# Optimization experiments

Measured on AMD Instinct MI355X. Metric: run time of the kernel, lower is better.

Reference implementation:

```python
import jax, jax.numpy as jnp
import numpy as np

T, D, N, K, H = 2048, 4096, 32, 8, 128
ROPE_THETA = 500000.0


def setup_inputs() -> dict:
    key = jax.random.key(0)
    ks = jax.random.split(key, 5)
    s = 0.02
    return {
        "x": jax.random.normal(ks[0], (T, D), jnp.float32) * s,
        "positions": jnp.arange(T, dtype=jnp.int64 if jax.config.jax_enable_x64 else jnp.int32),
        "Wq": jax.random.normal(ks[1], (D, N, H), jnp.float32) * s,
        "Wk": jax.random.normal(ks[2], (D, K, H), jnp.float32) * s,
        "Wv": jax.random.normal(ks[3], (D, K, H), jnp.float32) * s,
        "Wo": jax.random.normal(ks[4], (N, H, D), jnp.float32) * s,
    }


def _rope(positions, q, k):
    # positions: [T]; q: [T,N,H]; k: [T,K,H]. Half-split rotation (Llama style).
    half = H // 2
    inv_freq = 1.0 / (ROPE_THETA ** (jnp.arange(0, half, dtype=jnp.float32) / half))
    ang = positions.astype(jnp.float32)[:, None] * inv_freq  # [T, H/2]
    cos = jnp.cos(ang)[:, None, :]  # [T,1,H/2]
    sin = jnp.sin(ang)[:, None, :]

    def rot(x):
        x1, x2 = x[..., :half], x[..., half:]
        return jnp.concatenate([x1 * cos - x2 * sin, x2 * cos + x1 * sin], axis=-1)

    return rot(q), rot(k)


def reference(x, positions, Wq, Wk, Wv, Wo):
    q = jnp.einsum('td,dnh->tnh', x, Wq)  # [T,N,H]
    k = jnp.einsum('td,dkh->tkh', x, Wk)  # [T,K,H]
    v = jnp.einsum('td,dkh->tkh', x, Wv)
    q, k = _rope(positions, q, k)

    rep = N // K  # GQA: expand kv heads to query heads
    kr = jnp.repeat(k, rep, axis=1)  # [T,N,H]
    vr = jnp.repeat(v, rep, axis=1)

    scale = 1.0 / jnp.sqrt(jnp.asarray(H, jnp.float32))
    scores = jnp.einsum('tnh,snh->nts', q, kr) * scale  # [N,T,T]
    causal = positions[:, None] >= positions[None, :]   # [T,T]
    scores = jnp.where(causal[None, :, :], scores, jnp.finfo(scores.dtype).min)
    probs = jax.nn.softmax(scores, axis=-1)
    ctx = jnp.einsum('nts,snh->tnh', probs, vr)  # [T,N,H]
    return jnp.einsum('tnh,nhd->td', ctx, Wo)
```

## Files before the change

### kernel.cpp

```cpp
#include <hip/hip_runtime.h>
#include <hip/hip_bf16.h>

#define T_SEQ 2048
#define D_MODEL 4096
#define N_HEADS 32
#define K_HEADS 8
#define HEAD_DIM 128

typedef unsigned short u16;
typedef short sfrag8 __attribute__((ext_vector_type(8)));
typedef float ffrag4 __attribute__((ext_vector_type(4)));

#if defined(__has_builtin)
#  if __has_builtin(__builtin_amdgcn_exp2f)
#    define EXP2F(x) __builtin_amdgcn_exp2f(x)
#  else
#    define EXP2F(x) exp2f(x)
#  endif
#else
#  define EXP2F(x) exp2f(x)
#endif

#define QSCALE_LOG2E 0.12751744900463627f

__device__ __forceinline__ float bf2f(u16 u) {
    return __uint_as_float(((unsigned int)u) << 16);
}
__device__ __forceinline__ u16 f2bf(float f) {
    unsigned int x = __float_as_uint(f);
    unsigned int r = (x + 0x7fffu + ((x >> 16) & 1u)) >> 16;
    return (u16)r;
}
__device__ __forceinline__ uint4 pack8(const float4 a, const float4 b) {
    uint4 r;
    r.x = (unsigned)f2bf(a.x) | ((unsigned)f2bf(a.y) << 16);
    r.y = (unsigned)f2bf(a.z) | ((unsigned)f2bf(a.w) << 16);
    r.z = (unsigned)f2bf(b.x) | ((unsigned)f2bf(b.y) << 16);
    r.w = (unsigned)f2bf(b.z) | ((unsigned)f2bf(b.w) << 16);
    return r;
}

__device__ __forceinline__ void gload_lds16(const u16* g, u16* l) {
    __builtin_amdgcn_global_load_lds(
        (const __attribute__((address_space(1))) void*)g,
        (__attribute__((address_space(3))) void*)l, 16, 0, 0);
}

__global__ __launch_bounds__(256) void convert_bf16(
    const float* __restrict__ X, u16* __restrict__ Y, int n8)
{
    const int i = blockIdx.x * 256 + threadIdx.x;
    if (i < n8) {
        float4 a = ((const float4*)X)[(size_t)i * 2];
        float4 b = ((const float4*)X)[(size_t)i * 2 + 1];
        ((uint4*)Y)[i] = pack8(a, b);
    }
}

__global__ __launch_bounds__(256) void transpose_f32_bf16(
    const float* __restrict__ W, u16* __restrict__ WT, int R, int C)
{
    __shared__ float Ts[64][65];
    const int t = threadIdx.x;
    const int c0 = blockIdx.x * 64, r0 = blockIdx.y * 64;
    const int rl = t >> 4, cl = (t & 15) * 4;
#pragma unroll
    for (int p = 0; p < 4; ++p) {
        const int r = p * 16 + rl;
        float4 v = *(const float4*)(W + (size_t)(r0 + r) * C + c0 + cl);
        Ts[r][cl] = v.x; Ts[r][cl + 1] = v.y; Ts[r][cl + 2] = v.z; Ts[r][cl + 3] = v.w;
    }
    __syncthreads();
    const int nl = t >> 2, k4 = (t & 3) * 16;
    u16 tmp[16];
#pragma unroll
    for (int j = 0; j < 16; ++j) tmp[j] = f2bf(Ts[k4 + j][nl]);
    u16* dst = WT + (size_t)(c0 + nl) * R + r0 + k4;
    *(uint4*)(dst) = *(uint4*)&tmp[0];
    *(uint4*)(dst + 8) = *(uint4*)&tmp[8];
}

template <int CMODE>
__global__ __launch_bounds__(256) void gemm_bt(
    const u16* __restrict__ A, const u16* __restrict__ BT,
    void* __restrict__ Cp, int M, int Nb, int Kd, int ldc)
{
    __shared__ __align__(16) u16 As[128 * 64];
    __shared__ __align__(16) u16 Bs[128 * 64];

    const int tid = threadIdx.x;
    const int lane = tid & 63;
    const int w = tid >> 6;
    const int wm = w >> 1, wn = w & 1;
    const int ln = lane & 15, quad = lane >> 4;

    const int m0 = blockIdx.y * 128, n0 = blockIdx.x * 128;

    size_t aoff[4], boff[4];
#pragma unroll
    for (int i = 0; i < 4; ++i) {
        const int row = (i * 4 + w) * 8 + (lane >> 3);
        const int cg = (lane & 7) ^ (lane >> 3);
        aoff[i] = (size_t)(m0 + row) * Kd + cg * 8;
        boff[i] = (size_t)(n0 + row) * Kd + cg * 8;
    }

    ffrag4 acc[4][4];
#pragma unroll
    for (int mi = 0; mi < 4; ++mi)
#pragma unroll
        for (int ni = 0; ni < 4; ++ni) acc[mi][ni] = (ffrag4){0.f, 0.f, 0.f, 0.f};

    for (int k0 = 0; k0 < Kd; k0 += 64) {
#pragma unroll
        for (int i = 0; i < 4; ++i) {
            gload_lds16(A + aoff[i] + k0, &As[(i * 4 + w) * 512]);
            gload_lds16(BT + boff[i] + k0, &Bs[(i * 4 + w) * 512]);
        }
        __syncthreads();

#pragma unroll
        for (int kk = 0; kk < 2; ++kk) {
            sfrag8 af[4], bfv[4];
#pragma unroll
            for (int mi = 0; mi < 4; ++mi) {
                const int row = wm * 64 + mi * 16 + ln;
                const int pc = ((kk * 4) | quad) ^ (ln & 7);
                af[mi] = *(const sfrag8*)&As[row * 64 + pc * 8];
            }
#pragma unroll
            for (int ni = 0; ni < 4; ++ni) {
                const int row = wn * 64 + ni * 16 + ln;
                const int pc = ((kk * 4) | quad) ^ (ln & 7);
                bfv[ni] = *(const sfrag8*)&Bs[row * 64 + pc * 8];
            }
#pragma unroll
            for (int mi = 0; mi < 4; ++mi)
#pragma unroll
                for (int ni = 0; ni < 4; ++ni)
                    acc[mi][ni] = __builtin_amdgcn_mfma_f32_16x16x32_bf16(
                        af[mi], bfv[ni], acc[mi][ni], 0, 0, 0);
        }
        __syncthreads();
    }

#pragma unroll
    for (int mi = 0; mi < 4; ++mi) {
#pragma unroll
        for (int ni = 0; ni < 4; ++ni) {
            const int gcol = n0 + wn * 64 + ni * 16 + ln;
#pragma unroll
            for (int i = 0; i < 4; ++i) {
                const int grow = m0 + wm * 64 + mi * 16 + quad * 4 + i;
                if constexpr (CMODE == 1) {
                    ((float*)Cp)[(size_t)grow * ldc + gcol] = acc[mi][ni][i];
                } else if constexpr (CMODE == 3) {
                    if (gcol < 1024) {
                        ((u16*)Cp)[(size_t)grow * 1024 + gcol] = f2bf(acc[mi][ni][i]);
                    } else {
                        ((u16*)Cp + 2097152)[(size_t)(gcol - 1024) * T_SEQ + grow] =
                            f2bf(acc[mi][ni][i]);
                    }
                } else {
                    ((u16*)Cp)[(size_t)grow * ldc + gcol] = f2bf(acc[mi][ni][i]);
                }
            }
        }
    }
}

template <int AMODE, int CMODE>
__global__ __launch_bounds__(256) void gemm_any(
    const void* __restrict__ Ap, const float* __restrict__ B, void* __restrict__ Cp,
    int M, int Nb, int Kd, int ldc)
{
    __shared__ __align__(16) u16 As[64 * 64];
    __shared__ __align__(16) u16 Bs[64 * 72];

    const int tid = threadIdx.x;
    const int n0 = blockIdx.x * 64, m0 = blockIdx.y * 64;

    const int lr = tid >> 3;
    const int cc8 = tid & 7;
    const int sw = ((cc8 ^ (lr & 7)) * 8);
    const int dstA0 = lr * 64 + sw;
    const int dstA1 = (lr + 32) * 64 + sw;
    const size_t arow0 = (size_t)(m0 + lr) * Kd;
    const size_t arow1 = (size_t)(m0 + lr + 32) * Kd;

    const int kr = tid >> 2;
    const int ncb = (tid & 3) * 16;

    const int lane = tid & 63;
    const int w = tid >> 6;
    const int col16 = lane & 15;
    const int quad = lane >> 4;
    const int swl = lane & 7;
    const int mrow = w * 16 + col16;

    ffrag4 acc[4];
#pragma unroll
    for (int j = 0; j < 4; ++j) acc[j] = (ffrag4){0.f, 0.f, 0.f, 0.f};

    for (int k0 = 0; k0 < Kd; k0 += 64) {
        if constexpr (AMODE == 1) {
            const u16* Af = (const u16*)Ap;
            uint4 va0 = *(const uint4*)(Af + arow0 + k0 + cc8 * 8);
            uint4 va1 = *(const uint4*)(Af + arow1 + k0 + cc8 * 8);
            *(uint4*)&As[dstA0] = va0;
            *(uint4*)&As[dstA1] = va1;
        } else {
            const float* Af = (const float*)Ap;
            float4 a00 = *(const float4*)(Af + arow0 + k0 + cc8 * 8);
            float4 a01 = *(const float4*)(Af + arow0 + k0 + cc8 * 8 + 4);
            float4 a10 = *(const float4*)(Af + arow1 + k0 + cc8 * 8);
            float4 a11 = *(const float4*)(Af + arow1 + k0 + cc8 * 8 + 4);
            *(uint4*)&As[dstA0] = pack8(a00, a01);
            *(uint4*)&As[dstA1] = pack8(a10, a11);
        }
        {
            const float* bp = B + (size_t)(k0 + kr) * Nb + n0 + ncb;
            float4 b0 = *(const float4*)(bp);
            float4 b1 = *(const float4*)(bp + 4);
            float4 b2 = *(const float4*)(bp + 8);
            float4 b3 = *(const float4*)(bp + 12);
            u16 tmp[16];
            tmp[0] = f2bf(b0.x); tmp[1] = f2bf(b0.y); tmp[2] = f2bf(b0.z); tmp[3] = f2bf(b0.w);
            tmp[4] = f2bf(b1.x); tmp[5] = f2bf(b1.y); tmp[6] = f2bf(b1.z); tmp[7] = f2bf(b1.w);
            tmp[8] = f2bf(b2.x); tmp[9] = f2bf(b2.y); tmp[10] = f2bf(b2.z); tmp[11] = f2bf(b2.w);
            tmp[12] = f2bf(b3.x); tmp[13] = f2bf(b3.y); tmp[14] = f2bf(b3.z); tmp[15] = f2bf(b3.w);
#pragma unroll
            for (int e = 0; e < 16; ++e)
                Bs[(ncb + e) * 72 + kr] = tmp[e];
        }
        __syncthreads();
#pragma unroll
        for (int c = 0; c < 2; ++c) {
            const int cc = c * 4 + quad;
            const int koffA = (cc ^ swl) * 8;
            sfrag8 af = *(const sfrag8*)&As[mrow * 64 + koffA];
#pragma unroll
            for (int j = 0; j < 4; ++j) {
                sfrag8 bfv = *(const sfrag8*)&Bs[(j * 16 + col16) * 72 + cc * 8];
                acc[j] = __builtin_amdgcn_mfma_f32_16x16x32_bf16(af, bfv, acc[j], 0, 0, 0);
            }
        }
        __syncthreads();
    }

#pragma unroll
    for (int j = 0; j < 4; ++j) {
        const int gcol = n0 + j * 16 + col16;
#pragma unroll
        for (int i = 0; i < 4; ++i) {
            const int grow = m0 + w * 16 + quad * 4 + i;
            if constexpr (CMODE == 1) {
                ((float*)Cp)[(size_t)grow * ldc + gcol] = acc[j][i];
            } else if constexpr (CMODE == 2) {
                ((u16*)Cp)[(size_t)gcol * ldc + grow] = f2bf(acc[j][i]);
            } else {
                ((u16*)Cp)[(size_t)grow * ldc + gcol] = f2bf(acc[j][i]);
            }
        }
    }
}

__global__ __launch_bounds__(64) void rope_kernel(
    u16* __restrict__ buf, int nheads, int t0)
{
    const int h = blockIdx.x;
    const int t = blockIdx.y;
    u16* rowp = buf + ((size_t)t * nheads + h) * HEAD_DIM;
    const int i = threadIdx.x;
    const float p = (float)(t0 + t);
    const float inv = expf(-((float)i * (1.0f / 64.0f)) * 13.122363377404329f);
    const float ang = p * inv;
    const float c = cosf(ang);
    const float s = sinf(ang);
    const float x1 = bf2f(rowp[i]);
    const float x2 = bf2f(rowp[i + 64]);
    rowp[i] = f2bf(x1 * c - x2 * s);
    rowp[i + 64] = f2bf(x2 * c + x1 * s);
}

__global__ __launch_bounds__(256) void attn_mfma(
    const u16* q, const u16* __restrict__ k,
    const u16* __restrict__ vt, u16* ctx, int t0)
{
    __shared__ __align__(16) u16 Kt[64 * 136];
    __shared__ __align__(16) u16 Vt[128 * 72];
    __shared__ __align__(16) u16 Ps[4][16 * 72];

    const int head = blockIdx.x;
    const int qt = gridDim.y - 1 - blockIdx.y;
    const int kvh = head >> 2;
    const int tid = threadIdx.x;
    const int lane = tid & 63;
    const int w = tid >> 6;
    const int ln = lane & 15;
    const int quad = lane >> 4;

    const int kr = tid >> 2;
    const int c4 = (tid & 3) * 32;
    const int vd = tid >> 1;
    const int vh = (tid & 1) * 32;

    const int qrow_loc = qt * 64 + w * 16 + ln;
    sfrag8 qf[4];
    {
        const u16* qg = q + ((size_t)qrow_loc * N_HEADS + head) * HEAD_DIM;
#pragma unroll
        for (int kk = 0; kk < 4; ++kk)
            qf[kk] = *(const sfrag8*)(qg + kk * 32 + quad * 8);
    }

    ffrag4 acc_o[8];
#pragma unroll
    for (int dt = 0; dt < 8; ++dt) acc_o[dt] = (ffrag4){0.f, 0.f, 0.f, 0.f};
    float mrow[4] = {-INFINITY, -INFINITY, -INFINITY, -INFINITY};
    float lrow_l[4] = {0.f, 0.f, 0.f, 0.f};

    const int Tq0 = t0 + qt * 64;
    const int nst = Tq0 / 64 + 1;
    const int qabs_base = Tq0 + w * 16 + quad * 4;

    for (int st = 0; st < nst; ++st) {
        const int kv0 = st * 64;
        const bool diag = (st == nst - 1);

        __syncthreads();
        {
            const u16* kg = k + ((size_t)(kv0 + kr) * K_HEADS + kvh) * HEAD_DIM + c4;
            u16* kd = &Kt[kr * 136 + c4];
#pragma unroll
            for (int j = 0; j < 4; ++j)
                *(uint4*)(kd + j * 8) = *(const uint4*)(kg + j * 8);
        }
        {
            const u16* vg = vt + ((size_t)(kvh * 128 + vd)) * T_SEQ + kv0 + vh;
            u16* vdst = &Vt[vd * 72 + vh];
#pragma unroll
            for (int j = 0; j < 4; ++j)
                *(uint4*)(vdst + j * 8) = *(const uint4*)(vg + j * 8);
        }
        __syncthreads();

        const int ktc = diag ? ((w < 2) ? 2 : 4) : 4;
        ffrag4 sacc[4];
        __builtin_amdgcn_s_setprio(1);
#pragma unroll
        for (int kt = 0; kt < 4; ++kt) {
            if (kt >= ktc) break;
            sacc[kt] = (ffrag4){0.f, 0.f, 0.f, 0.f};
#pragma unroll
            for (int kk = 0; kk < 4; ++kk) {
                sfrag8 bfr = *(const sfrag8*)&Kt[(kt * 16 + ln) * 136 + kk * 32 + quad * 8];
                sacc[kt] = __builtin_amdgcn_mfma_f32_16x16x32_bf16(qf[kk], bfr, sacc[kt], 0, 0, 0);
            }
        }
        __builtin_amdgcn_s_setprio(0);
        float sv[4][4];
#pragma unroll
        for (int kt = 0; kt < 4; ++kt) {
            if (kt >= ktc) break;
            const int key_abs = kv0 + kt * 16 + ln;
#pragma unroll
            for (int i = 0; i < 4; ++i) {
                float s = sacc[kt][i] * QSCALE_LOG2E;
                if (diag && key_abs > qabs_base + i) s = -INFINITY;
                sv[kt][i] = s;
            }
        }
        float tm[4];
#pragma unroll
        for (int i = 0; i < 4; ++i) {
            float t = sv[0][i];
            for (int kt = 1; kt < ktc; ++kt) t = fmaxf(t, sv[kt][i]);
            t = fmaxf(t, __shfl_xor(t, 1));
            t = fmaxf(t, __shfl_xor(t, 2));
            t = fmaxf(t, __shfl_xor(t, 4));
            t = fmaxf(t, __shfl_xor(t, 8));
            tm[i] = t;
        }
        float alpha[4];
#pragma unroll
        for (int i = 0; i < 4; ++i) {
            const float mn = fmaxf(mrow[i], tm[i]);
            alpha[i] = EXP2F(mrow[i] - mn);
            mrow[i] = mn;
        }
        const bool noop = (alpha[0] == 1.f) && (alpha[1] == 1.f) &&
                          (alpha[2] == 1.f) && (alpha[3] == 1.f);
        if (!__all(noop)) {
#pragma unroll
            for (int i = 0; i < 4; ++i) {
                lrow_l[i] *= alpha[i];
#pragma unroll
                for (int dt = 0; dt < 8; ++dt) acc_o[dt][i] *= alpha[i];
            }
        }
#pragma unroll
        for (int kt = 0; kt < 4; ++kt) {
            if (kt >= ktc) break;
#pragma unroll
            for (int i = 0; i < 4; ++i) {
                const float p = EXP2F(sv[kt][i] - mrow[i]);
                lrow_l[i] += p;
                Ps[w][(quad * 4 + i) * 72 + kt * 16 + ln] = f2bf(p);
            }
        }
        const int kbm = ktc >> 1;
        __builtin_amdgcn_s_setprio(1);
#pragma unroll
        for (int kb = 0; kb < 2; ++kb) {
            if (kb >= kbm) break;
            sfrag8 afr = *(const sfrag8*)&Ps[w][ln * 72 + kb * 32 + quad * 8];
#pragma unroll
            for (int dt = 0; dt < 8; ++dt) {
                sfrag8 bfr = *(const sfrag8*)&Vt[(dt * 16 + ln) * 72 + kb * 32 + quad * 8];
                acc_o[dt] = __builtin_amdgcn_mfma_f32_16x16x32_bf16(afr, bfr, acc_o[dt], 0, 0, 0);
            }
        }
        __builtin_amdgcn_s_setprio(0);
    }

    float invl[4];
#pragma unroll
    for (int i = 0; i < 4; ++i) {
        float t = lrow_l[i];
        t += __shfl_xor(t, 1);
        t += __shfl_xor(t, 2);
        t += __shfl_xor(t, 4);
        t += __shfl_xor(t, 8);
        invl[i] = 1.0f / t;
    }
#pragma unroll
    for (int i = 0; i < 4; ++i) {
        u16* og = ctx + ((size_t)(qt * 64 + w * 16 + quad * 4 + i) * N_HEADS + head) * HEAD_DIM;
#pragma unroll
        for (int dt = 0; dt < 8; ++dt)
            og[dt * 16 + ln] = f2bf(acc_o[dt][i] * invl[i]);
    }
}

extern "C" void kernel_launch(void* const* d_in, const int* in_sizes, int n_in,
                              void* d_out, int out_size, void* d_ws, size_t ws_size,
                              hipStream_t stream) {
    (void)in_sizes; (void)n_in; (void)out_size;
    const float* x  = (const float*)d_in[0];
    const float* Wq = (const float*)d_in[2];
    const float* Wk = (const float*)d_in[3];
    const float* Wv = (const float*)d_in[4];
    const float* Wo = (const float*)d_in[5];
    float* out = (float*)d_out;
    char* ws = (char*)d_ws;
    const size_t MiB = 1024 * 1024;

    if (ws_size >= 88 * MiB) {
        u16* kbuf  = (u16*)(ws);
        u16* vtbuf = (u16*)(ws + 4 * MiB);
        u16* qsl   = (u16*)(ws + 8 * MiB);
        u16* xb    = (u16*)(ws + 24 * MiB);
        u16* WkT   = (u16*)(ws + 40 * MiB);
        u16* WvT   = (u16*)(ws + 48 * MiB);
        u16* WshT  = (u16*)(ws + 56 * MiB);

        convert_bf16<<<dim3(T_SEQ * D_MODEL / 8 / 256), 256, 0, stream>>>(
            x, xb, T_SEQ * D_MODEL / 8);
        transpose_f32_bf16<<<dim3(16, 64), 256, 0, stream>>>(
            Wk, WkT, D_MODEL, K_HEADS * HEAD_DIM);
        transpose_f32_bf16<<<dim3(16, 64), 256, 0, stream>>>(
            Wv, WvT, D_MODEL, K_HEADS * HEAD_DIM);
        transpose_f32_bf16<<<dim3(64, 64), 256, 0, stream>>>(
            Wq, WshT, D_MODEL, N_HEADS * HEAD_DIM);

        gemm_bt<3><<<dim3(16, 16), 256, 0, stream>>>(
            xb, WkT, kbuf, T_SEQ, 2048, D_MODEL, 0);
        rope_kernel<<<dim3(K_HEADS, T_SEQ), 64, 0, stream>>>(kbuf, K_HEADS, 0);

        gemm_bt<0><<<dim3(32, 16), 256, 0, stream>>>(
            xb, WshT, qsl, T_SEQ, N_HEADS * HEAD_DIM, D_MODEL, N_HEADS * HEAD_DIM);
        rope_kernel<<<dim3(N_HEADS, T_SEQ), 64, 0, stream>>>(qsl, N_HEADS, 0);

        attn_mfma<<<dim3(N_HEADS, T_SEQ / 64), 256, 0, stream>>>(
            qsl, kbuf, vtbuf, qsl, 0);

        transpose_f32_bf16<<<dim3(64, 64), 256, 0, stream>>>(
            Wo, WshT, N_HEADS * HEAD_DIM, D_MODEL);
        gemm_bt<1><<<dim3(32, 16), 256, 0, stream>>>(
            qsl, WshT, out, T_SEQ, D_MODEL, N_HEADS * HEAD_DIM, D_MODEL);
        return;
    }

    u16* kbuf  = (u16*)(ws);
    u16* vtbuf = (u16*)(ws + 4194304);
    u16* qsl   = (u16*)(ws + 8388608);

    int S = 8;
    if (ws_size >= (size_t)8388608 + 16777216)      S = 1;
    else if (ws_size >= (size_t)8388608 + 8388608)  S = 2;
    else if (ws_size >= (size_t)8388608 + 4194304)  S = 4;
    const int Ts = T_SEQ / S;

    gemm_any<0, 0><<<dim3(16, T_SEQ / 64), 256, 0, stream>>>(
        x, Wk, kbuf, T_SEQ, K_HEADS * HEAD_DIM, D_MODEL, K_HEADS * HEAD_DIM);
    gemm_any<0, 2><<<dim3(16, T_SEQ / 64), 256, 0, stream>>>(
        x, Wv, vtbuf, T_SEQ, K_HEADS * HEAD_DIM, D_MODEL, T_SEQ);
    rope_kernel<<<dim3(K_HEADS, T_SEQ), 64, 0, stream>>>(kbuf, K_HEADS, 0);

    for (int s = 0; s < S; ++s) {
        const int t0 = s * Ts;
        gemm_any<0, 0><<<dim3(64, Ts / 64), 256, 0, stream>>>(
            x + (size_t)t0 * D_MODEL, Wq, qsl, Ts, D_MODEL, D_MODEL, D_MODEL);
        rope_kernel<<<dim3(N_HEADS, Ts), 64, 0, stream>>>(qsl, N_HEADS, t0);
        attn_mfma<<<dim3(N_HEADS, Ts / 64), 256, 0, stream>>>(
            qsl, kbuf, vtbuf, qsl, t0);
        gemm_any<1, 1><<<dim3(64, Ts / 64), 256, 0, stream>>>(
            qsl, Wo, out + (size_t)t0 * D_MODEL, Ts, D_MODEL, N_HEADS * HEAD_DIM, D_MODEL);
    }
}
```

Baseline: 607.3 us.

## Fuse QKV projections into one GEMM, remap workgroups per XCD, lazy softmax rescale

Concatenates transposed Wq, Wk and Wv into one weight buffer and runs a single GEMM whose epilogue routes columns to the Q, K and transposed V buffers. This removes a launch and improves wave fill. Adds a workgroup-id remap that groups consecutive tiles onto the same XCD to improve L2 reuse. In attention, the row-max reduction and accumulator rescale are skipped unless some score exceeds the running max by more than 8 (log2 units). This trades extra dynamic range in the unnormalized exponentials for fewer shuffles and rescales.

```diff
diff --git a/kernel.cpp b/kernel.cpp
--- a/kernel.cpp
+++ b/kernel.cpp
@@ -94,7 +94,14 @@
     const int wm = w >> 1, wn = w & 1;
     const int ln = lane & 15, quad = lane >> 4;
 
-    const int m0 = blockIdx.y * 128, n0 = blockIdx.x * 128;
+    int wid = blockIdx.y * gridDim.x + blockIdx.x;
+    const int nwg = gridDim.x * gridDim.y;
+    const int cpx = nwg >> 3;
+    wid = (wid & 7) * cpx + (wid >> 3);
+    const int bx = wid % gridDim.x;
+    const int by = wid / gridDim.x;
+
+    const int m0 = by * 128, n0 = bx * 128;
 
     size_t aoff[4], boff[4];
 #pragma unroll
@@ -154,12 +161,15 @@
                 const int grow = m0 + wm * 64 + mi * 16 + quad * 4 + i;
                 if constexpr (CMODE == 1) {
                     ((float*)Cp)[(size_t)grow * ldc + gcol] = acc[mi][ni][i];
-                } else if constexpr (CMODE == 3) {
-                    if (gcol < 1024) {
-                        ((u16*)Cp)[(size_t)grow * 1024 + gcol] = f2bf(acc[mi][ni][i]);
+                } else if constexpr (CMODE == 4) {
+                    u16* base = (u16*)Cp;
+                    const u16 v = f2bf(acc[mi][ni][i]);
+                    if (gcol < 4096) {
+                        base[4194304u + (size_t)grow * 4096 + gcol] = v;
+                    } else if (gcol < 5120) {
+                        base[(size_t)grow * 1024 + (gcol - 4096)] = v;
                     } else {
-                        ((u16*)Cp + 2097152)[(size_t)(gcol - 1024) * T_SEQ + grow] =
-                            f2bf(acc[mi][ni][i]);
+                        base[2097152u + (size_t)(gcol - 5120) * T_SEQ + grow] = v;
                     }
                 } else {
                     ((u16*)Cp)[(size_t)grow * ldc + gcol] = f2bf(acc[mi][ni][i]);
@@ -371,32 +381,42 @@
                 sv[kt][i] = s;
             }
         }
-        float tm[4];
-#pragma unroll
-        for (int i = 0; i < 4; ++i) {
-            float t = sv[0][i];
-            for (int kt = 1; kt < ktc; ++kt) t = fmaxf(t, sv[kt][i]);
-            t = fmaxf(t, __shfl_xor(t, 1));
-            t = fmaxf(t, __shfl_xor(t, 2));
-            t = fmaxf(t, __shfl_xor(t, 4));
-            t = fmaxf(t, __shfl_xor(t, 8));
-            tm[i] = t;
-        }
-        float alpha[4];
-#pragma unroll
-        for (int i = 0; i < 4; ++i) {
-            const float mn = fmaxf(mrow[i], tm[i]);
-            alpha[i] = EXP2F(mrow[i] - mn);
-            mrow[i] = mn;
-        }
-        const bool noop = (alpha[0] == 1.f) && (alpha[1] == 1.f) &&
-                          (alpha[2] == 1.f) && (alpha[3] == 1.f);
-        if (!__all(noop)) {
+        bool grew = false;
+#pragma unroll
+        for (int kt = 0; kt < 4; ++kt) {
+            if (kt >= ktc) break;
+#pragma unroll
+            for (int i = 0; i < 4; ++i)
+                grew |= (sv[kt][i] > mrow[i] + 8.0f);
+        }
+        if (__any(grew)) {
+            float tm[4];
 #pragma unroll
             for (int i = 0; i < 4; ++i) {
-                lrow_l[i] *= alpha[i];
-#pragma unroll
-                for (int dt = 0; dt < 8; ++dt) acc_o[dt][i] *= alpha[i];
+                float t = sv[0][i];
+                for (int kt = 1; kt < ktc; ++kt) t = fmaxf(t, sv[kt][i]);
+                t = fmaxf(t, __shfl_xor(t, 1));
+                t = fmaxf(t, __shfl_xor(t, 2));
+                t = fmaxf(t, __shfl_xor(t, 4));
+                t = fmaxf(t, __shfl_xor(t, 8));
+                tm[i] = t;
+            }
+            float alpha[4];
+#pragma unroll
+            for (int i = 0; i < 4; ++i) {
+                const float mn = fmaxf(mrow[i], tm[i]);
+                alpha[i] = EXP2F(mrow[i] - mn);
+                mrow[i] = mn;
+            }
+            const bool noop = (alpha[0] == 1.f) && (alpha[1] == 1.f) &&
+                              (alpha[2] == 1.f) && (alpha[3] == 1.f);
+            if (!__all(noop)) {
+#pragma unroll
+                for (int i = 0; i < 4; ++i) {
+                    lrow_l[i] *= alpha[i];
+#pragma unroll
+                    for (int dt = 0; dt < 8; ++dt) acc_o[dt][i] *= alpha[i];
+                }
             }
         }
 #pragma unroll
@@ -461,34 +481,30 @@
         u16* vtbuf = (u16*)(ws + 4 * MiB);
         u16* qsl   = (u16*)(ws + 8 * MiB);
         u16* xb    = (u16*)(ws + 24 * MiB);
-        u16* WkT   = (u16*)(ws + 40 * MiB);
-        u16* WvT   = (u16*)(ws + 48 * MiB);
-        u16* WshT  = (u16*)(ws + 56 * MiB);
+        u16* WqkvT = (u16*)(ws + 40 * MiB);
 
         convert_bf16<<<dim3(T_SEQ * D_MODEL / 8 / 256), 256, 0, stream>>>(
             x, xb, T_SEQ * D_MODEL / 8);
+        transpose_f32_bf16<<<dim3(64, 64), 256, 0, stream>>>(
+            Wq, WqkvT, D_MODEL, N_HEADS * HEAD_DIM);
         transpose_f32_bf16<<<dim3(16, 64), 256, 0, stream>>>(
-            Wk, WkT, D_MODEL, K_HEADS * HEAD_DIM);
+            Wk, WqkvT + (size_t)4096 * 4096, D_MODEL, K_HEADS * HEAD_DIM);
         transpose_f32_bf16<<<dim3(16, 64), 256, 0, stream>>>(
-            Wv, WvT, D_MODEL, K_HEADS * HEAD_DIM);
-        transpose_f32_bf16<<<dim3(64, 64), 256, 0, stream>>>(
-            Wq, WshT, D_MODEL, N_HEADS * HEAD_DIM);
-
-        gemm_bt<3><<<dim3(16, 16), 256, 0, stream>>>(
-            xb, WkT, kbuf, T_SEQ, 2048, D_MODEL, 0);
+            Wv, WqkvT + (size_t)5120 * 4096, D_MODEL, K_HEADS * HEAD_DIM);
+
+        gemm_bt<4><<<dim3(48, 16), 256, 0, stream>>>(
+            xb, WqkvT, ws, T_SEQ, 6144, D_MODEL, 0);
+
         rope_kernel<<<dim3(K_HEADS, T_SEQ), 64, 0, stream>>>(kbuf, K_HEADS, 0);
-
-        gemm_bt<0><<<dim3(32, 16), 256, 0, stream>>>(
-            xb, WshT, qsl, T_SEQ, N_HEADS * HEAD_DIM, D_MODEL, N_HEADS * HEAD_DIM);
         rope_kernel<<<dim3(N_HEADS, T_SEQ), 64, 0, stream>>>(qsl, N_HEADS, 0);
 
         attn_mfma<<<dim3(N_HEADS, T_SEQ / 64), 256, 0, stream>>>(
             qsl, kbuf, vtbuf, qsl, 0);
 
         transpose_f32_bf16<<<dim3(64, 64), 256, 0, stream>>>(
-            Wo, WshT, N_HEADS * HEAD_DIM, D_MODEL);
+            Wo, WqkvT, N_HEADS * HEAD_DIM, D_MODEL);
         gemm_bt<1><<<dim3(32, 16), 256, 0, stream>>>(
-            qsl, WshT, out, T_SEQ, D_MODEL, N_HEADS * HEAD_DIM, D_MODEL);
+            qsl, WqkvT, out, T_SEQ, D_MODEL, N_HEADS * HEAD_DIM, D_MODEL);
         return;
     }
 
```

Result: faster. 549.7 us (-9.5%).
